# Kernel optimization log

Hardware: AMD Instinct MI355X
Metric: run time of the kernel (lower is better)

Reference implementation:

```python
import jax, jax.numpy as jnp
import numpy as np

N_HEADS = 64 * 4 // 32  # 8 heads, head_dim 32
LN_EPS = 1e-5


def conv3d(x, w, b):
    # x: [B,C,D,H,W], w: [O,I,3,3,3], padding=1 == SAME for k=3
    y = jax.lax.conv_general_dilated(
        x, w, window_strides=(1, 1, 1), padding='SAME',
        dimension_numbers=('NCDHW', 'OIDHW', 'NCDHW'))
    return y + b[None, :, None, None, None]


def layer_norm(x, g, b):
    m = jnp.mean(x, axis=-1, keepdims=True)
    v = jnp.var(x, axis=-1, keepdims=True)  # biased var, as torch LayerNorm
    return (x - m) * jax.lax.rsqrt(v + LN_EPS) * g + b


def linear(x, w, b):
    # torch Linear layout: w [out, in]
    return jnp.einsum('bsi,oi->bso', x, w) + b


def setup_inputs() -> dict:
    key = jax.random.key(0)
    ks = jax.random.split(key, 16)
    C_in, d = 64, 256
    x = jax.random.normal(ks[0], (1, C_in, 16, 16, 16), dtype=jnp.float32)
    s = 0.02
    params = {
        'conv1_w': jax.random.normal(ks[1], (d, C_in, 3, 3, 3), jnp.float32) * s,
        'conv1_b': jnp.zeros((d,), jnp.float32),
        'ln_g': jnp.ones((d,), jnp.float32),
        'ln_b': jnp.zeros((d,), jnp.float32),
        'q_w': jax.random.normal(ks[2], (d, d), jnp.float32) * s,
        'q_b': jnp.zeros((d,), jnp.float32),
        'k_w': jax.random.normal(ks[3], (d, d), jnp.float32) * s,
        'k_b': jnp.zeros((d,), jnp.float32),
        'v_w': jax.random.normal(ks[4], (d, d), jnp.float32) * s,
        'v_b': jnp.zeros((d,), jnp.float32),
        'ffn_w': jax.random.normal(ks[5], (d, d), jnp.float32) * s,
        'ffn_b': jnp.zeros((d,), jnp.float32),
        'conv2_w': jax.random.normal(ks[6], (C_in, d, 3, 3, 3), jnp.float32) * s,
        'conv2_b': jnp.zeros((C_in,), jnp.float32),
    }
    return {'x': x, **params}


def reference(x, conv1_w, conv1_b, ln_g, ln_b, q_w, q_b, k_w, k_b, v_w, v_b,
              ffn_w, ffn_b, conv2_w, conv2_b):
    B, _, D, H, W = x.shape
    S = D * H * W
    # PositionalEmbedding: conv3d then flatten; the learned pos-emb is a
    # freshly-initialized zeros Parameter in the original => no-op add.
    h0 = conv3d(x, conv1_w, conv1_b)              # [B, d, D, H, W]
    d_model = h0.shape[1]
    h0 = h0.reshape(B, d_model, S).transpose(0, 2, 1)  # [B, S, d]

    hn = layer_norm(h0, ln_g, ln_b)
    hd = d_model // N_HEADS

    def split_heads(t):
        return t.reshape(B, S, N_HEADS, hd).transpose(0, 2, 1, 3)  # [B, nH, S, hd]

    q = split_heads(linear(hn, q_w, q_b))
    k = split_heads(linear(hn, k_w, k_b))
    v = split_heads(linear(hn, v_w, v_b))

    scores = jnp.einsum('bhqd,bhkd->bhqk', q, k) / jnp.sqrt(
        jnp.asarray(hd, q.dtype))
    # NOTE: original uses nn.Softmax(dim=2) -> normalize over QUERY axis
    attn = jax.nn.softmax(scores, axis=2)
    out = jnp.einsum('bhqk,bhkd->bhqd', attn, v)  # [B, nH, S, hd]
    out = out.transpose(0, 2, 1, 3).reshape(B, S, d_model)

    xt = out + hn                                  # residual onto NORMED input
    h2 = layer_norm(xt, ln_g, ln_b)                # same LN weights reused
    h3 = jax.nn.relu(linear(h2, ffn_w, ffn_b)) + xt

    h3 = h3.transpose(0, 2, 1).reshape(B, d_model, D, H, W)
    return conv3d(h3, conv2_w, conv2_b)
```

## Files before the change

### kernel.cpp

```cpp
#include <hip/hip_runtime.h>
#include <math.h>

#define S 4096
#define DM 256

using short8 = __attribute__((ext_vector_type(8))) short;
using short4v = __attribute__((ext_vector_type(4))) short;
using f32x4 = __attribute__((ext_vector_type(4))) float;
using f32x16 = __attribute__((ext_vector_type(16))) float;

static constexpr float QK_SCALE_LOG2E = 0.17677669529663687f * 1.4426950408889634f;

__device__ __forceinline__ short f2bf(float f) {
  union { float f; unsigned u; } v;
  v.f = f;
  unsigned r = (v.u + 0x7FFFu + ((v.u >> 16) & 1u)) >> 16;
  return (short)r;
}

__device__ __forceinline__ float bf2f(short s) {
  union { unsigned u; float f; } v;
  v.u = ((unsigned)(unsigned short)s) << 16;
  return v.f;
}

__device__ __forceinline__ unsigned cvt_pk_bf16(float lo, float hi) {
  unsigned r;
  asm("v_cvt_pk_bf16_f32 %0, %1, %2" : "=v"(r) : "v"(lo), "v"(hi));
  return r;
}

__device__ __forceinline__ float fexp2(float x) {
  float r;
  asm("v_exp_f32 %0, %1" : "=v"(r) : "v"(x));
  return r;
}

__device__ __forceinline__ int pad_idx(int s) {
  int d = s >> 8, h = (s >> 4) & 15, w = s & 15;
  return ((d + 1) * 18 + (h + 1)) * 18 + (w + 1);
}

__global__ __launch_bounds__(256) void k_prep(const float* __restrict__ x,
                                              const float* __restrict__ c1w,
                                              const float* __restrict__ c2w,
                                              const float* __restrict__ qw,
                                              const float* __restrict__ kw,
                                              const float* __restrict__ vw,
                                              const float* __restrict__ fw,
                                              short* __restrict__ xpad,
                                              short* __restrict__ w1t,
                                              short* __restrict__ w2t,
                                              short* __restrict__ wqkvf,
                                              short* __restrict__ hpad) {
  int bid = blockIdx.x, tid = threadIdx.x;
  if (bid < 1458) {
    int idx = bid * 256 + tid;
    int row = idx >> 6, c = idx & 63;
    int pd = row / 324, rem = row - pd * 324;
    int ph = rem / 18, pw = rem - ph * 18;
    short v = 0;
    if ((unsigned)(pd - 1) < 16u && (unsigned)(ph - 1) < 16u && (unsigned)(pw - 1) < 16u) {
      int s = (pd - 1) * 256 + (ph - 1) * 16 + (pw - 1);
      v = f2bf(x[c * 4096 + s]);
    }
    xpad[idx] = v;
  } else if (bid < 3186) {
    int idx = (bid - 1458) * 256 + tid;
    int o = idx / 1728, r = idx - o * 1728;
    int off = r >> 6, ic = r & 63;
    w1t[idx] = f2bf(c1w[(o * 64 + ic) * 27 + off]);
  } else if (bid < 4914) {
    int idx = (bid - 3186) * 256 + tid;
    int o = idx / 6912, r = idx - o * 6912;
    int off = r >> 8, ic = r & 255;
    w2t[idx] = f2bf(c2w[(o * 256 + ic) * 27 + off]);
  } else if (bid < 5938) {
    int idx = (bid - 4914) * 256 + tid;
    int which = idx >> 16, r = idx & 65535;
    const float* src = (which == 0) ? qw : (which == 1) ? kw : (which == 2) ? vw : fw;
    wqkvf[idx] = f2bf(src[r]);
  } else {
    int i = (bid - 5938) * 2048 + tid * 8;
    short8 z = {0, 0, 0, 0, 0, 0, 0, 0};
    *(short8*)(hpad + i) = z;
  }
}

__global__ __launch_bounds__(256) void k_conv1m(const short* __restrict__ xpad,
                                                const short* __restrict__ wt,
                                                const float* __restrict__ bias,
                                                float* __restrict__ h0) {
  int bid = blockIdx.x;
  int mt2 = bid >> 1, ch = bid & 1;
  int tid = threadIdx.x, w = tid >> 6, lane = tid & 63, g = lane >> 4, c = lane & 15;
  int d = mt2 >> 3, h = (mt2 & 7) * 2;
  int nb = ch * 128 + w * 32;
  f32x4 accA0 = {}, accA1 = {}, accB0 = {}, accB1 = {};
  for (int off = 0; off < 27; ++off) {
    int kd = off / 9, r = off - kd * 9, kh = r / 3, kw = r - kh * 3;
    int rowb = ((d + kd) * 18 + h + kh) * 18 + kw + c;
#pragma unroll
    for (int kc = 0; kc < 2; ++kc) {
      short8 afA = *(const short8*)(xpad + rowb * 64 + kc * 32 + 8 * g);
      short8 afB = *(const short8*)(xpad + (rowb + 18) * 64 + kc * 32 + 8 * g);
      int kidx = off * 64 + kc * 32 + 8 * g;
      short8 b0 = *(const short8*)(wt + (nb + c) * 1728 + kidx);
      short8 b1 = *(const short8*)(wt + (nb + 16 + c) * 1728 + kidx);
      accA0 = __builtin_amdgcn_mfma_f32_16x16x32_bf16(afA, b0, accA0, 0, 0, 0);
      accA1 = __builtin_amdgcn_mfma_f32_16x16x32_bf16(afA, b1, accA1, 0, 0, 0);
      accB0 = __builtin_amdgcn_mfma_f32_16x16x32_bf16(afB, b0, accB0, 0, 0, 0);
      accB1 = __builtin_amdgcn_mfma_f32_16x16x32_bf16(afB, b1, accB1, 0, 0, 0);
    }
  }
  int o0 = nb + c, o1 = nb + 16 + c;
  float bv0 = bias[o0], bv1 = bias[o1];
  int sA = mt2 * 32 + 4 * g;
#pragma unroll
  for (int i = 0; i < 4; ++i) {
    h0[(sA + i) * 256 + o0] = accA0[i] + bv0;
    h0[(sA + i) * 256 + o1] = accA1[i] + bv1;
    h0[(sA + 16 + i) * 256 + o0] = accB0[i] + bv0;
    h0[(sA + 16 + i) * 256 + o1] = accB1[i] + bv1;
  }
}

__global__ __launch_bounds__(256) void k_layernorm(const float* __restrict__ in,
                                                   const float* __restrict__ g,
                                                   const float* __restrict__ b,
                                                   float* __restrict__ outf,
                                                   short* __restrict__ outb) {
  int s = blockIdx.x, tid = threadIdx.x;
  float xv = in[s * 256 + tid];
  float s1 = xv, s2 = xv * xv;
#pragma unroll
  for (int off = 32; off > 0; off >>= 1) {
    s1 += __shfl_down(s1, off);
    s2 += __shfl_down(s2, off);
  }
  __shared__ float w1[4], w2[4], mb[2];
  int wid = tid >> 6;
  if ((tid & 63) == 0) { w1[wid] = s1; w2[wid] = s2; }
  __syncthreads();
  if (tid == 0) {
    float t1 = w1[0] + w1[1] + w1[2] + w1[3];
    float t2 = w2[0] + w2[1] + w2[2] + w2[3];
    float m = t1 * (1.f / 256.f);
    float var = t2 * (1.f / 256.f) - m * m;
    mb[0] = m;
    mb[1] = rsqrtf(var + 1e-5f);
  }
  __syncthreads();
  float y = (xv - mb[0]) * mb[1] * g[tid] + b[tid];
  outf[s * 256 + tid] = y;
  outb[s * 256 + tid] = f2bf(y);
}

__global__ __launch_bounds__(256) void k_gemm_qkv(const short* __restrict__ ab,
                                                  const short* __restrict__ wqb,
                                                  const short* __restrict__ wkb,
                                                  const short* __restrict__ wvb,
                                                  const float* __restrict__ qbi,
                                                  const float* __restrict__ kbi,
                                                  const float* __restrict__ vbi,
                                                  short* __restrict__ qb,
                                                  short* __restrict__ kb,
                                                  short* __restrict__ vt) {
  int y = blockIdx.y;
  const short* wb = (y == 0) ? wqb : ((y == 1) ? wkb : wvb);
  int tid = threadIdx.x, w = tid >> 6, lane = tid & 63, g = lane >> 4, c = lane & 15;
  int m0 = blockIdx.x * 16;
  int nb = w * 64;
  f32x4 acc[4];
#pragma unroll
  for (int n = 0; n < 4; ++n) acc[n] = {0.f, 0.f, 0.f, 0.f};
#pragma unroll 2
  for (int k0 = 0; k0 < 256; k0 += 32) {
    short8 af = *(const short8*)(ab + (m0 + c) * 256 + k0 + 8 * g);
#pragma unroll
    for (int n = 0; n < 4; ++n) {
      short8 bf = *(const short8*)(wb + (nb + 16 * n + c) * 256 + k0 + 8 * g);
      acc[n] = __builtin_amdgcn_mfma_f32_16x16x32_bf16(af, bf, acc[n], 0, 0, 0);
    }
  }
  if (y < 2) {
    const float* bi = (y == 0) ? qbi : kbi;
    float sc = (y == 0) ? QK_SCALE_LOG2E : 1.f;
    short* ob = (y == 0) ? qb : kb;
#pragma unroll
    for (int n = 0; n < 4; ++n) {
      int o = nb + 16 * n + c;
      float bv = bi[o];
      int hh = o >> 5, dj = o & 31;
#pragma unroll
      for (int i = 0; i < 4; ++i) {
        int s = m0 + 4 * g + i;
        ob[((size_t)hh * S + s) * 32 + dj] = f2bf((acc[n][i] + bv) * sc);
      }
    }
  } else {
#pragma unroll
    for (int n = 0; n < 4; ++n) {
      int o = nb + 16 * n + c;
      float bv = vbi[o];
      short4v st;
#pragma unroll
      for (int i = 0; i < 4; ++i) st[i] = f2bf(acc[n][i] + bv);
      *(short4v*)(vt + (size_t)o * S + m0 + 4 * g) = st;
    }
  }
}

__global__ __launch_bounds__(256) void k_attn1(const short* __restrict__ qb,
                                               const short* __restrict__ kb,
                                               float* __restrict__ lpart) {
  int bid = blockIdx.x;
  int h = bid & 7;
  int rest = bid >> 3;
  int kt = rest >> 3, qs = rest & 7;
  int tid = threadIdx.x;
  int w = tid >> 6, lane = tid & 63;
  int lo = lane & 31, hi = lane >> 5;
  int k0 = kt * 128 + w * 32;
  const size_t hb = (size_t)h * S;
  const short* krow = kb + (hb + k0 + lo) * 32;
  short8 ak0 = *(const short8*)(krow + 8 * hi);
  short8 ak1 = *(const short8*)(krow + 16 + 8 * hi);
  f32x16 ls = {};
  const f32x16 z16 = {};
  int qend = qs * 512 + 512;
  for (int q0 = qs * 512; q0 < qend; q0 += 32) {
    short8 bq0 = *(const short8*)(qb + (hb + q0 + lo) * 32 + 8 * hi);
    short8 bq1 = *(const short8*)(qb + (hb + q0 + lo) * 32 + 16 + 8 * hi);
    __builtin_amdgcn_s_setprio(1);
    f32x16 p = __builtin_amdgcn_mfma_f32_32x32x16_bf16(ak0, bq0, z16, 0, 0, 0);
    p = __builtin_amdgcn_mfma_f32_32x32x16_bf16(ak1, bq1, p, 0, 0, 0);
    __builtin_amdgcn_s_setprio(0);
#pragma unroll
    for (int r = 0; r < 16; ++r) ls[r] += fexp2(p[r]);
  }
#pragma unroll
  for (int r = 0; r < 16; ++r) {
    float v = ls[r];
    v += __shfl_xor(v, 1);
    v += __shfl_xor(v, 2);
    v += __shfl_xor(v, 4);
    v += __shfl_xor(v, 8);
    v += __shfl_xor(v, 16);
    ls[r] = v;
  }
  if (lo == 0) {
#pragma unroll
    for (int r = 0; r < 16; ++r)
      lpart[qs * 32768 + h * 4096 + k0 + (r & 3) + 8 * (r >> 2) + 4 * hi] = ls[r];
  }
}

__global__ __launch_bounds__(256) void k_scalevt(short* __restrict__ vt,
                                                 const float* __restrict__ lpart) {
  int idx = blockIdx.x * 256 + threadIdx.x;
  int row = idx >> 9;
  int col0 = (idx & 511) << 3;
  int h = row >> 5;
  const float* lp = lpart + h * 4096 + col0;
  float4 s0 = {0.f, 0.f, 0.f, 0.f}, s1 = {0.f, 0.f, 0.f, 0.f};
#pragma unroll
  for (int j = 0; j < 8; ++j) {
    float4 a = *(const float4*)(lp + j * 32768);
    float4 b = *(const float4*)(lp + j * 32768 + 4);
    s0.x += a.x; s0.y += a.y; s0.z += a.z; s0.w += a.w;
    s1.x += b.x; s1.y += b.y; s1.z += b.z; s1.w += b.w;
  }
  float4 l0, l1;
  l0.x = 1.f / s0.x; l0.y = 1.f / s0.y; l0.z = 1.f / s0.z; l0.w = 1.f / s0.w;
  l1.x = 1.f / s1.x; l1.y = 1.f / s1.y; l1.z = 1.f / s1.z; l1.w = 1.f / s1.w;
  short8 v = *(short8*)(vt + (size_t)row * S + col0);
  union { unsigned u[4]; short8 s8; } r;
  r.u[0] = cvt_pk_bf16(bf2f(v[0]) * l0.x, bf2f(v[1]) * l0.y);
  r.u[1] = cvt_pk_bf16(bf2f(v[2]) * l0.z, bf2f(v[3]) * l0.w);
  r.u[2] = cvt_pk_bf16(bf2f(v[4]) * l1.x, bf2f(v[5]) * l1.y);
  r.u[3] = cvt_pk_bf16(bf2f(v[6]) * l1.z, bf2f(v[7]) * l1.w);
  *(short8*)(vt + (size_t)row * S + col0) = r.s8;
}

__global__ __launch_bounds__(256, 4) void k_attn2(const short* __restrict__ qb,
                                                  const short* __restrict__ kb,
                                                  const short* __restrict__ vt,
                                                  short* __restrict__ parts) {
  int bid = blockIdx.x;
  int h = bid & 7;
  int rest = bid >> 3;
  int qt = rest >> 3, ks = rest & 7;
  int tid = threadIdx.x;
  int w = tid >> 6, lane = tid & 63;
  int lo = lane & 31, hi = lane >> 5;
  int sl = lo ^ ((((lo >> 2) ^ (lo >> 3)) & 1) * 12);
  int q0a = qt * 256 + w * 64;
  int q0b = q0a + 32;
  const size_t hb = (size_t)h * S;
  short8 bqa0 = *(const short8*)(qb + (hb + q0a + lo) * 32 + 8 * hi);
  short8 bqa1 = *(const short8*)(qb + (hb + q0a + lo) * 32 + 16 + 8 * hi);
  short8 bqb0 = *(const short8*)(qb + (hb + q0b + lo) * 32 + 8 * hi);
  short8 bqb1 = *(const short8*)(qb + (hb + q0b + lo) * 32 + 16 + 8 * hi);
  f32x16 accA = {}, accB = {};
  const short* krow = kb + (hb + sl) * 32;
  const short* vrow = vt + ((size_t)(h * 32) + lo) * S;
  const f32x16 z16 = {};
  int k0 = ks * 512;
  short8 ak0 = *(const short8*)(krow + (size_t)k0 * 32 + 8 * hi);
  short8 ak1 = *(const short8*)(krow + (size_t)k0 * 32 + 16 + 8 * hi);
#pragma unroll 1
  for (int it = 0; it < 16; ++it) {
    int kn = k0 + 32;
    short8 nak0 = *(const short8*)(krow + (size_t)kn * 32 + 8 * hi);
    short8 nak1 = *(const short8*)(krow + (size_t)kn * 32 + 16 + 8 * hi);
    short8 bv0 = *(const short8*)(vrow + k0 + 8 * hi);
    short8 bv1 = *(const short8*)(vrow + k0 + 16 + 8 * hi);
    __builtin_amdgcn_s_setprio(1);
    f32x16 pA = __builtin_amdgcn_mfma_f32_32x32x16_bf16(ak0, bqa0, z16, 0, 0, 0);
    f32x16 pB = __builtin_amdgcn_mfma_f32_32x32x16_bf16(ak0, bqb0, z16, 0, 0, 0);
    pA = __builtin_amdgcn_mfma_f32_32x32x16_bf16(ak1, bqa1, pA, 0, 0, 0);
    pB = __builtin_amdgcn_mfma_f32_32x32x16_bf16(ak1, bqb1, pB, 0, 0, 0);
    __builtin_amdgcn_s_setprio(0);
    union { unsigned u[4]; short8 s8; } fA0, fA1, fB0, fB1;
#pragma unroll
    for (int m = 0; m < 4; ++m)
      fA0.u[m] = cvt_pk_bf16(fexp2(pA[2 * m]), fexp2(pA[2 * m + 1]));
#pragma unroll
    for (int m = 0; m < 4; ++m)
      fA1.u[m] = cvt_pk_bf16(fexp2(pA[8 + 2 * m]), fexp2(pA[9 + 2 * m]));
#pragma unroll
    for (int m = 0; m < 4; ++m)
      fB0.u[m] = cvt_pk_bf16(fexp2(pB[2 * m]), fexp2(pB[2 * m + 1]));
#pragma unroll
    for (int m = 0; m < 4; ++m)
      fB1.u[m] = cvt_pk_bf16(fexp2(pB[8 + 2 * m]), fexp2(pB[9 + 2 * m]));
    __builtin_amdgcn_s_setprio(1);
    accA = __builtin_amdgcn_mfma_f32_32x32x16_bf16(fA0.s8, bv0, accA, 0, 0, 0);
    accB = __builtin_amdgcn_mfma_f32_32x32x16_bf16(fB0.s8, bv0, accB, 0, 0, 0);
    accA = __builtin_amdgcn_mfma_f32_32x32x16_bf16(fA1.s8, bv1, accA, 0, 0, 0);
    accB = __builtin_amdgcn_mfma_f32_32x32x16_bf16(fB1.s8, bv1, accB, 0, 0, 0);
    __builtin_amdgcn_s_setprio(0);
    ak0 = nak0;
    ak1 = nak1;
    k0 = kn;
  }
  short* part = parts + (size_t)ks * (S * DM);
  int col = h * 32 + lo;
#pragma unroll
  for (int r = 0; r < 16; ++r) {
    int qrel = (r & 3) + 8 * (r >> 2) + 4 * hi;
    part[(q0a + qrel) * 256 + col] = f2bf(accA[r]);
    part[(q0b + qrel) * 256 + col] = f2bf(accB[r]);
  }
}

__global__ __launch_bounds__(256) void k_combine_ln(const short* __restrict__ parts,
                                                    const float* __restrict__ hn,
                                                    const float* __restrict__ g,
                                                    const float* __restrict__ b,
                                                    float* __restrict__ xt,
                                                    short* __restrict__ h2b) {
  int s = blockIdx.x, tid = threadIdx.x;
  int i = s * 256 + tid;
  const int SD4 = S * DM;
  float xv = hn[i];
#pragma unroll
  for (int j = 0; j < 8; ++j) xv += bf2f(parts[i + j * SD4]);
  xt[i] = xv;
  float s1 = xv, s2 = xv * xv;
#pragma unroll
  for (int off = 32; off > 0; off >>= 1) {
    s1 += __shfl_down(s1, off);
    s2 += __shfl_down(s2, off);
  }
  __shared__ float w1[4], w2[4], mb[2];
  int wid = tid >> 6;
  if ((tid & 63) == 0) { w1[wid] = s1; w2[wid] = s2; }
  __syncthreads();
  if (tid == 0) {
    float t1 = w1[0] + w1[1] + w1[2] + w1[3];
    float t2 = w2[0] + w2[1] + w2[2] + w2[3];
    float m = t1 * (1.f / 256.f);
    float var = t2 * (1.f / 256.f) - m * m;
    mb[0] = m;
    mb[1] = rsqrtf(var + 1e-5f);
  }
  __syncthreads();
  h2b[i] = f2bf((xv - mb[0]) * mb[1] * g[tid] + b[tid]);
}

__global__ __launch_bounds__(256) void k_gemm_ffn(const short* __restrict__ ab,
                                                  const short* __restrict__ wb,
                                                  const float* __restrict__ bi,
                                                  const float* __restrict__ xt,
                                                  short* __restrict__ hpad) {
  int tid = threadIdx.x, w = tid >> 6, lane = tid & 63, g = lane >> 4, c = lane & 15;
  int m0 = blockIdx.x * 16;
  int nb = w * 64;
  f32x4 acc[4];
#pragma unroll
  for (int n = 0; n < 4; ++n) acc[n] = {0.f, 0.f, 0.f, 0.f};
#pragma unroll 2
  for (int k0 = 0; k0 < 256; k0 += 32) {
    short8 af = *(const short8*)(ab + (m0 + c) * 256 + k0 + 8 * g);
#pragma unroll
    for (int n = 0; n < 4; ++n) {
      short8 bf = *(const short8*)(wb + (nb + 16 * n + c) * 256 + k0 + 8 * g);
      acc[n] = __builtin_amdgcn_mfma_f32_16x16x32_bf16(af, bf, acc[n], 0, 0, 0);
    }
  }
  int pr[4];
#pragma unroll
  for (int i = 0; i < 4; ++i) pr[i] = pad_idx(m0 + 4 * g + i) * 256;
#pragma unroll
  for (int n = 0; n < 4; ++n) {
    int o = nb + 16 * n + c;
    float bv = bi[o];
#pragma unroll
    for (int i = 0; i < 4; ++i) {
      int s = m0 + 4 * g + i;
      float v = acc[n][i] + bv;
      v = v > 0.f ? v : 0.f;
      hpad[pr[i] + o] = f2bf(v + xt[s * 256 + o]);
    }
  }
}

__global__ __launch_bounds__(256) void k_conv2m(const short* __restrict__ hpad,
                                                const short* __restrict__ wt,
                                                float* __restrict__ pbase) {
  __shared__ float red[3][32][65];
  int bid = blockIdx.x;
  int mt2 = bid >> 2, kh = bid & 3;
  int tid = threadIdx.x, w = tid >> 6, lane = tid & 63, g = lane >> 4, c = lane & 15;
  int d = mt2 >> 3, h = (mt2 & 7) * 2;
  f32x4 accA[4], accB[4];
#pragma unroll
  for (int n = 0; n < 4; ++n) { accA[n] = {0.f, 0.f, 0.f, 0.f}; accB[n] = {0.f, 0.f, 0.f, 0.f}; }
  int off0 = kh * 7;
  int offn = (kh == 3) ? 6 : 7;
  for (int off = off0 + w; off < off0 + offn; off += 4) {
    int kd = off / 9, rr = off - kd * 9, kkh = rr / 3, kw = rr - kkh * 3;
    int rowb = ((d + kd) * 18 + h + kkh) * 18 + kw + c;
    const short* arowA = hpad + rowb * 256;
    const short* arowB = hpad + (rowb + 18) * 256;
    const short* wrow = wt + off * 256;
#pragma unroll 2
    for (int kc = 0; kc < 8; ++kc) {
      short8 afA = *(const short8*)(arowA + kc * 32 + 8 * g);
      short8 afB = *(const short8*)(arowB + kc * 32 + 8 * g);
#pragma unroll
      for (int n = 0; n < 4; ++n) {
        short8 bf = *(const short8*)(wrow + (16 * n + c) * 6912 + kc * 32 + 8 * g);
        accA[n] = __builtin_amdgcn_mfma_f32_16x16x32_bf16(afA, bf, accA[n], 0, 0, 0);
        accB[n] = __builtin_amdgcn_mfma_f32_16x16x32_bf16(afB, bf, accB[n], 0, 0, 0);
      }
    }
  }
  if (w > 0) {
#pragma unroll
    for (int n = 0; n < 4; ++n)
#pragma unroll
      for (int i = 0; i < 4; ++i) {
        red[w - 1][n * 4 + i][lane] = accA[n][i];
        red[w - 1][16 + n * 4 + i][lane] = accB[n][i];
      }
  }
  __syncthreads();
  if (w == 0) {
    float* pbuf = pbase + (size_t)kh * (S * DM / 4);
#pragma unroll
    for (int n = 0; n < 4; ++n) {
      int o = 16 * n + c;
      float4 stA, stB;
#pragma unroll
      for (int i = 0; i < 4; ++i) {
        float a = accA[n][i] + red[0][n * 4 + i][lane] + red[1][n * 4 + i][lane] + red[2][n * 4 + i][lane];
        float bb = accB[n][i] + red[0][16 + n * 4 + i][lane] + red[1][16 + n * 4 + i][lane] + red[2][16 + n * 4 + i][lane];
        ((float*)&stA)[i] = a;
        ((float*)&stB)[i] = bb;
      }
      *(float4*)(pbuf + o * 4096 + mt2 * 32 + 4 * g) = stA;
      *(float4*)(pbuf + o * 4096 + mt2 * 32 + 16 + 4 * g) = stB;
    }
  }
}

__global__ __launch_bounds__(256) void k_conv2fin(const float* __restrict__ pbase,
                                                  const float* __restrict__ bias,
                                                  float* __restrict__ out) {
  int idx4 = (blockIdx.x * 256 + threadIdx.x) * 4;
  int o = idx4 >> 12;
  const int PS = S * DM / 4;
  float4 a = *(const float4*)(pbase + idx4);
  float4 b = *(const float4*)(pbase + PS + idx4);
  float4 c = *(const float4*)(pbase + 2 * PS + idx4);
  float4 d = *(const float4*)(pbase + 3 * PS + idx4);
  float bv = bias[o];
  float4 r;
  r.x = a.x + b.x + c.x + d.x + bv;
  r.y = a.y + b.y + c.y + d.y + bv;
  r.z = a.z + b.z + c.z + d.z + bv;
  r.w = a.w + b.w + c.w + d.w + bv;
  *(float4*)(out + idx4) = r;
}

extern "C" void kernel_launch(void* const* d_in, const int* in_sizes, int n_in,
                              void* d_out, int out_size, void* d_ws, size_t ws_size,
                              hipStream_t stream) {
  const float* x   = (const float*)d_in[0];
  const float* c1w = (const float*)d_in[1];
  const float* c1b = (const float*)d_in[2];
  const float* lng = (const float*)d_in[3];
  const float* lnb = (const float*)d_in[4];
  const float* qw  = (const float*)d_in[5];
  const float* qbi = (const float*)d_in[6];
  const float* kw  = (const float*)d_in[7];
  const float* kbi = (const float*)d_in[8];
  const float* vw  = (const float*)d_in[9];
  const float* vbi = (const float*)d_in[10];
  const float* fw  = (const float*)d_in[11];
  const float* fbi = (const float*)d_in[12];
  const float* c2w = (const float*)d_in[13];
  const float* c2b = (const float*)d_in[14];
  float* out = (float*)d_out;
  float* ws = (float*)d_ws;

  const size_t SD = (size_t)S * DM;
  float* hn     = ws;
  float* xt     = hn + SD;
  short* partsb = (short*)(xt + SD);
  float* h0     = (float*)partsb;
  float* c2p    = (float*)partsb;
  float* lpart  = (float*)(partsb + 8 * SD);
  float* linv   = lpart + 262144;
  short* hnb    = (short*)(linv + 32768);
  short* h2b    = hnb + SD;
  short* qb     = h2b + SD;
  short* kb     = qb + SD;
  short* vt     = kb + SD;
  short* xpad   = vt + SD;
  short* hpad   = xpad + 373248;
  short* w1t    = hpad + 1492992;
  short* w2t    = w1t + 442368;
  short* wqb    = w2t + 442368;
  short* wkb    = wqb + 65536;
  short* wvb    = wkb + 65536;
  short* wfb    = wvb + 65536;

  k_prep<<<6667, 256, 0, stream>>>(x, c1w, c2w, qw, kw, vw, fw,
                                   xpad, w1t, w2t, wqb, hpad);

  k_conv1m<<<256, 256, 0, stream>>>(xpad, w1t, c1b, h0);
  k_layernorm<<<4096, 256, 0, stream>>>(h0, lng, lnb, hn, hnb);

  k_gemm_qkv<<<dim3(256, 3), 256, 0, stream>>>(hnb, wqb, wkb, wvb, qbi, kbi, vbi,
                                               qb, kb, vt);

  k_attn1<<<2048, 256, 0, stream>>>(qb, kb, lpart);
  k_scalevt<<<1024, 256, 0, stream>>>(vt, lpart);
  k_attn2<<<1024, 256, 0, stream>>>(qb, kb, vt, partsb);
  k_combine_ln<<<4096, 256, 0, stream>>>(partsb, hn, lng, lnb, xt, h2b);

  k_gemm_ffn<<<256, 256, 0, stream>>>(h2b, wfb, fbi, xt, hpad);
  k_conv2m<<<512, 256, 0, stream>>>(hpad, w2t, c2p);
  k_conv2fin<<<256, 256, 0, stream>>>(c2p, c2b, out);
}
```

Before: 151.0 us.

## Fuse conv1 with LayerNorm and transpose conv weights through LDS

Conv1 is retiled so each block computes all 256 output channels for 16 spatial rows. This lets the LayerNorm mean and variance be reduced in-block and applied before writing hn/hnb, which removes the separate LayerNorm kernel and the fp32 h0 round trip. Weight prep now uses one block per output channel that reads the source contiguously and transposes through shared memory, cutting the prep grid size. The cost is less reuse of each A fragment per block (16 rows instead of 32) and fewer blocks in conv1, since one block now covers 16 rows by 256 channels.

Result: slower. 154.2 us (+2.1%).

```diff
diff --git a/kernel.cpp b/kernel.cpp
--- a/kernel.cpp
+++ b/kernel.cpp
@@ -53,6 +53,7 @@
                                               short* __restrict__ w2t,
                                               short* __restrict__ wqkvf,
                                               short* __restrict__ hpad) {
+  __shared__ short tlds[6912];
   int bid = blockIdx.x, tid = threadIdx.x;
   if (bid < 1458) {
     int idx = bid * 256 + tid;
@@ -65,95 +66,114 @@
       v = f2bf(x[c * 4096 + s]);
     }
     xpad[idx] = v;
-  } else if (bid < 3186) {
-    int idx = (bid - 1458) * 256 + tid;
-    int o = idx / 1728, r = idx - o * 1728;
-    int off = r >> 6, ic = r & 63;
-    w1t[idx] = f2bf(c1w[(o * 64 + ic) * 27 + off]);
-  } else if (bid < 4914) {
-    int idx = (bid - 3186) * 256 + tid;
-    int o = idx / 6912, r = idx - o * 6912;
-    int off = r >> 8, ic = r & 255;
-    w2t[idx] = f2bf(c2w[(o * 256 + ic) * 27 + off]);
-  } else if (bid < 5938) {
-    int idx = (bid - 4914) * 256 + tid;
+  } else if (bid < 1714) {
+    int o = bid - 1458;
+    const float* src = c1w + o * 1728;
+    for (int t = tid; t < 1728; t += 256) {
+      int ic = t / 27, off = t - ic * 27;
+      tlds[off * 64 + ic] = f2bf(src[t]);
+    }
+    __syncthreads();
+    for (int u = tid; u < 1728; u += 256) w1t[o * 1728 + u] = tlds[u];
+  } else if (bid < 1778) {
+    int o = bid - 1714;
+    const float* src = c2w + o * 6912;
+    for (int t = tid; t < 6912; t += 256) {
+      int ic = t / 27, off = t - ic * 27;
+      tlds[off * 256 + ic] = f2bf(src[t]);
+    }
+    __syncthreads();
+    for (int u = tid; u < 6912; u += 256) w2t[o * 6912 + u] = tlds[u];
+  } else if (bid < 2802) {
+    int idx = (bid - 1778) * 256 + tid;
     int which = idx >> 16, r = idx & 65535;
     const float* src = (which == 0) ? qw : (which == 1) ? kw : (which == 2) ? vw : fw;
     wqkvf[idx] = f2bf(src[r]);
   } else {
-    int i = (bid - 5938) * 2048 + tid * 8;
+    int i = (bid - 2802) * 2048 + tid * 8;
     short8 z = {0, 0, 0, 0, 0, 0, 0, 0};
     *(short8*)(hpad + i) = z;
   }
 }
 
-__global__ __launch_bounds__(256) void k_conv1m(const short* __restrict__ xpad,
-                                                const short* __restrict__ wt,
-                                                const float* __restrict__ bias,
-                                                float* __restrict__ h0) {
-  int bid = blockIdx.x;
-  int mt2 = bid >> 1, ch = bid & 1;
+__global__ __launch_bounds__(256) void k_conv1ln(const short* __restrict__ xpad,
+                                                 const short* __restrict__ wt,
+                                                 const float* __restrict__ bias,
+                                                 const float* __restrict__ lng,
+                                                 const float* __restrict__ lnb,
+                                                 float* __restrict__ hn,
+                                                 short* __restrict__ hnb) {
+  __shared__ float red1[4][16], red2[4][16];
+  __shared__ float mstd[16][2];
+  int mt = blockIdx.x;
   int tid = threadIdx.x, w = tid >> 6, lane = tid & 63, g = lane >> 4, c = lane & 15;
-  int d = mt2 >> 3, h = (mt2 & 7) * 2;
-  int nb = ch * 128 + w * 32;
-  f32x4 accA0 = {}, accA1 = {}, accB0 = {}, accB1 = {};
+  int d = mt >> 4, h = mt & 15;
+  int nb = w * 64;
+  f32x4 acc[4];
+#pragma unroll
+  for (int n = 0; n < 4; ++n) acc[n] = {0.f, 0.f, 0.f, 0.f};
   for (int off = 0; off < 27; ++off) {
     int kd = off / 9, r = off - kd * 9, kh = r / 3, kw = r - kh * 3;
     int rowb = ((d + kd) * 18 + h + kh) * 18 + kw + c;
 #pragma unroll
     for (int kc = 0; kc < 2; ++kc) {
-      short8 afA = *(const short8*)(xpad + rowb * 64 + kc * 32 + 8 * g);
-      short8 afB = *(const short8*)(xpad + (rowb + 18) * 64 + kc * 32 + 8 * g);
+      short8 af = *(const short8*)(xpad + rowb * 64 + kc * 32 + 8 * g);
       int kidx = off * 64 + kc * 32 + 8 * g;
-      short8 b0 = *(const short8*)(wt + (nb + c) * 1728 + kidx);
-      short8 b1 = *(const short8*)(wt + (nb + 16 + c) * 1728 + kidx);
-      accA0 = __builtin_amdgcn_mfma_f32_16x16x32_bf16(afA, b0, accA0, 0, 0, 0);
-      accA1 = __builtin_amdgcn_mfma_f32_16x16x32_bf16(afA, b1, accA1, 0, 0, 0);
-      accB0 = __builtin_amdgcn_mfma_f32_16x16x32_bf16(afB, b0, accB0, 0, 0, 0);
-      accB1 = __builtin_amdgcn_mfma_f32_16x16x32_bf16(afB, b1, accB1, 0, 0, 0);
-    }
-  }
-  int o0 = nb + c, o1 = nb + 16 + c;
-  float bv0 = bias[o0], bv1 = bias[o1];
-  int sA = mt2 * 32 + 4 * g;
+#pragma unroll
+      for (int n = 0; n < 4; ++n) {
+        short8 bf = *(const short8*)(wt + (nb + 16 * n + c) * 1728 + kidx);
+        acc[n] = __builtin_amdgcn_mfma_f32_16x16x32_bf16(af, bf, acc[n], 0, 0, 0);
+      }
+    }
+  }
+  float s1[4] = {0.f, 0.f, 0.f, 0.f}, s2[4] = {0.f, 0.f, 0.f, 0.f};
+#pragma unroll
+  for (int n = 0; n < 4; ++n) {
+    float bv = bias[nb + 16 * n + c];
+#pragma unroll
+    for (int i = 0; i < 4; ++i) {
+      acc[n][i] += bv;
+      s1[i] += acc[n][i];
+      s2[i] += acc[n][i] * acc[n][i];
+    }
+  }
 #pragma unroll
   for (int i = 0; i < 4; ++i) {
-    h0[(sA + i) * 256 + o0] = accA0[i] + bv0;
-    h0[(sA + i) * 256 + o1] = accA1[i] + bv1;
-    h0[(sA + 16 + i) * 256 + o0] = accB0[i] + bv0;
-    h0[(sA + 16 + i) * 256 + o1] = accB1[i] + bv1;
-  }
-}
-
-__global__ __launch_bounds__(256) void k_layernorm(const float* __restrict__ in,
-                                                   const float* __restrict__ g,
-                                                   const float* __restrict__ b,
-                                                   float* __restrict__ outf,
-                                                   short* __restrict__ outb) {
-  int s = blockIdx.x, tid = threadIdx.x;
-  float xv = in[s * 256 + tid];
-  float s1 = xv, s2 = xv * xv;
-#pragma unroll
-  for (int off = 32; off > 0; off >>= 1) {
-    s1 += __shfl_down(s1, off);
-    s2 += __shfl_down(s2, off);
-  }
-  __shared__ float w1[4], w2[4], mb[2];
-  int wid = tid >> 6;
-  if ((tid & 63) == 0) { w1[wid] = s1; w2[wid] = s2; }
+    s1[i] += __shfl_xor(s1[i], 1); s2[i] += __shfl_xor(s2[i], 1);
+    s1[i] += __shfl_xor(s1[i], 2); s2[i] += __shfl_xor(s2[i], 2);
+    s1[i] += __shfl_xor(s1[i], 4); s2[i] += __shfl_xor(s2[i], 4);
+    s1[i] += __shfl_xor(s1[i], 8); s2[i] += __shfl_xor(s2[i], 8);
+  }
+  if (c == 0) {
+#pragma unroll
+    for (int i = 0; i < 4; ++i) {
+      red1[w][4 * g + i] = s1[i];
+      red2[w][4 * g + i] = s2[i];
+    }
+  }
   __syncthreads();
-  if (tid == 0) {
-    float t1 = w1[0] + w1[1] + w1[2] + w1[3];
-    float t2 = w2[0] + w2[1] + w2[2] + w2[3];
+  if (tid < 16) {
+    float t1 = red1[0][tid] + red1[1][tid] + red1[2][tid] + red1[3][tid];
+    float t2 = red2[0][tid] + red2[1][tid] + red2[2][tid] + red2[3][tid];
     float m = t1 * (1.f / 256.f);
     float var = t2 * (1.f / 256.f) - m * m;
-    mb[0] = m;
-    mb[1] = rsqrtf(var + 1e-5f);
+    mstd[tid][0] = m;
+    mstd[tid][1] = rsqrtf(var + 1e-5f);
   }
   __syncthreads();
-  float y = (xv - mb[0]) * mb[1] * g[tid] + b[tid];
-  outf[s * 256 + tid] = y;
-  outb[s * 256 + tid] = f2bf(y);
+  int s0 = mt * 16;
+#pragma unroll
+  for (int n = 0; n < 4; ++n) {
+    int o = nb + 16 * n + c;
+    float gg = lng[o], bb = lnb[o];
+#pragma unroll
+    for (int i = 0; i < 4; ++i) {
+      int row = 4 * g + i;
+      float y = (acc[n][i] - mstd[row][0]) * mstd[row][1] * gg + bb;
+      hn[(s0 + row) * 256 + o] = y;
+      hnb[(s0 + row) * 256 + o] = f2bf(y);
+    }
+  }
 }
 
 __global__ __launch_bounds__(256) void k_gemm_qkv(const short* __restrict__ ab,
@@ -531,7 +551,6 @@
   float* hn     = ws;
   float* xt     = hn + SD;
   short* partsb = (short*)(xt + SD);
-  float* h0     = (float*)partsb;
   float* c2p    = (float*)partsb;
   float* lpart  = (float*)(partsb + 8 * SD);
   float* linv   = lpart + 262144;
@@ -549,11 +568,10 @@
   short* wvb    = wkb + 65536;
   short* wfb    = wvb + 65536;
 
-  k_prep<<<6667, 256, 0, stream>>>(x, c1w, c2w, qw, kw, vw, fw,
+  k_prep<<<3531, 256, 0, stream>>>(x, c1w, c2w, qw, kw, vw, fw,
                                    xpad, w1t, w2t, wqb, hpad);
 
-  k_conv1m<<<256, 256, 0, stream>>>(xpad, w1t, c1b, h0);
-  k_layernorm<<<4096, 256, 0, stream>>>(h0, lng, lnb, hn, hnb);
+  k_conv1ln<<<256, 256, 0, stream>>>(xpad, w1t, c1b, lng, lnb, hn, hnb);
 
   k_gemm_qkv<<<dim3(256, 3), 256, 0, stream>>>(hnb, wqb, wkb, wvb, qbi, kbi, vbi,
                                                qb, kb, vt);
```

## Fuse layernorms into QKV and FFN GEMMs and transpose conv weights via LDS

Applied to the files above, without the earlier changes.

Drops the standalone layernorm and combine-layernorm kernels. The QKV GEMM now computes LN1 from h0 into swizzled LDS before its MFMA loop. A new FFN kernel recomputes LN1, adds the 8 attention partials, applies LN2 and keeps xt in LDS for the residual. Conv weight reordering in the prep kernel now goes through an LDS transpose with one block per output channel, which cuts the prep grid size. This removes two launches and the fp32/bf16 round-trips of hn, xt, hnb and h2b, at the cost of recomputing LN1 three times per row across QKV blocks and once more in the FFN kernel.

Result: faster. 143.2 us (-5.2%).

```diff
diff --git a/kernel.cpp b/kernel.cpp
--- a/kernel.cpp
+++ b/kernel.cpp
@@ -53,6 +53,7 @@
                                               short* __restrict__ w2t,
                                               short* __restrict__ wqkvf,
                                               short* __restrict__ hpad) {
+  __shared__ short tlds[7128];
   int bid = blockIdx.x, tid = threadIdx.x;
   if (bid < 1458) {
     int idx = bid * 256 + tid;
@@ -65,23 +66,37 @@
       v = f2bf(x[c * 4096 + s]);
     }
     xpad[idx] = v;
-  } else if (bid < 3186) {
-    int idx = (bid - 1458) * 256 + tid;
-    int o = idx / 1728, r = idx - o * 1728;
-    int off = r >> 6, ic = r & 63;
-    w1t[idx] = f2bf(c1w[(o * 64 + ic) * 27 + off]);
-  } else if (bid < 4914) {
-    int idx = (bid - 3186) * 256 + tid;
-    int o = idx / 6912, r = idx - o * 6912;
-    int off = r >> 8, ic = r & 255;
-    w2t[idx] = f2bf(c2w[(o * 256 + ic) * 27 + off]);
-  } else if (bid < 5938) {
-    int idx = (bid - 4914) * 256 + tid;
+  } else if (bid < 1714) {
+    int o = bid - 1458;
+    const float* src = c1w + o * 1728;
+    for (int t = tid; t < 1728; t += 256) {
+      int ic = t / 27, off = t - ic * 27;
+      tlds[off * 72 + ic] = f2bf(src[t]);
+    }
+    __syncthreads();
+    for (int u = tid; u < 1728; u += 256) {
+      int off = u >> 6, ic = u & 63;
+      w1t[o * 1728 + u] = tlds[off * 72 + ic];
+    }
+  } else if (bid < 1778) {
+    int o = bid - 1714;
+    const float* src = c2w + o * 6912;
+    for (int t = tid; t < 6912; t += 256) {
+      int ic = t / 27, off = t - ic * 27;
+      tlds[off * 264 + ic] = f2bf(src[t]);
+    }
+    __syncthreads();
+    for (int u = tid; u < 6912; u += 256) {
+      int off = u >> 8, ic = u & 255;
+      w2t[o * 6912 + u] = tlds[off * 264 + ic];
+    }
+  } else if (bid < 2802) {
+    int idx = (bid - 1778) * 256 + tid;
     int which = idx >> 16, r = idx & 65535;
     const float* src = (which == 0) ? qw : (which == 1) ? kw : (which == 2) ? vw : fw;
     wqkvf[idx] = f2bf(src[r]);
   } else {
-    int i = (bid - 5938) * 2048 + tid * 8;
+    int i = (bid - 2802) * 2048 + tid * 8;
     short8 z = {0, 0, 0, 0, 0, 0, 0, 0};
     *(short8*)(hpad + i) = z;
   }
@@ -125,38 +140,9 @@
   }
 }
 
-__global__ __launch_bounds__(256) void k_layernorm(const float* __restrict__ in,
-                                                   const float* __restrict__ g,
-                                                   const float* __restrict__ b,
-                                                   float* __restrict__ outf,
-                                                   short* __restrict__ outb) {
-  int s = blockIdx.x, tid = threadIdx.x;
-  float xv = in[s * 256 + tid];
-  float s1 = xv, s2 = xv * xv;
-#pragma unroll
-  for (int off = 32; off > 0; off >>= 1) {
-    s1 += __shfl_down(s1, off);
-    s2 += __shfl_down(s2, off);
-  }
-  __shared__ float w1[4], w2[4], mb[2];
-  int wid = tid >> 6;
-  if ((tid & 63) == 0) { w1[wid] = s1; w2[wid] = s2; }
-  __syncthreads();
-  if (tid == 0) {
-    float t1 = w1[0] + w1[1] + w1[2] + w1[3];
-    float t2 = w2[0] + w2[1] + w2[2] + w2[3];
-    float m = t1 * (1.f / 256.f);
-    float var = t2 * (1.f / 256.f) - m * m;
-    mb[0] = m;
-    mb[1] = rsqrtf(var + 1e-5f);
-  }
-  __syncthreads();
-  float y = (xv - mb[0]) * mb[1] * g[tid] + b[tid];
-  outf[s * 256 + tid] = y;
-  outb[s * 256 + tid] = f2bf(y);
-}
-
-__global__ __launch_bounds__(256) void k_gemm_qkv(const short* __restrict__ ab,
+__global__ __launch_bounds__(256) void k_gemm_qkv(const float* __restrict__ h0,
+                                                  const float* __restrict__ lng,
+                                                  const float* __restrict__ lnb,
                                                   const short* __restrict__ wqb,
                                                   const short* __restrict__ wkb,
                                                   const short* __restrict__ wvb,
@@ -166,17 +152,62 @@
                                                   short* __restrict__ qb,
                                                   short* __restrict__ kb,
                                                   short* __restrict__ vt) {
+  __shared__ short h2l[4096];
+  int m0 = blockIdx.x * 16;
+  int tid = threadIdx.x;
+  {
+    int r = tid >> 4, cg = tid & 15;
+    int row = m0 + r;
+    float u[16];
+    const float* hp = h0 + row * 256 + cg * 16;
+#pragma unroll
+    for (int i = 0; i < 16; i += 4) {
+      float4 a = *(const float4*)(hp + i);
+      u[i] = a.x; u[i + 1] = a.y; u[i + 2] = a.z; u[i + 3] = a.w;
+    }
+    float s1 = 0.f, s2 = 0.f;
+#pragma unroll
+    for (int i = 0; i < 16; ++i) { s1 += u[i]; s2 += u[i] * u[i]; }
+    s1 += __shfl_xor(s1, 1); s2 += __shfl_xor(s2, 1);
+    s1 += __shfl_xor(s1, 2); s2 += __shfl_xor(s2, 2);
+    s1 += __shfl_xor(s1, 4); s2 += __shfl_xor(s2, 4);
+    s1 += __shfl_xor(s1, 8); s2 += __shfl_xor(s2, 8);
+    float m = s1 * (1.f / 256.f);
+    float rstd = rsqrtf(s2 * (1.f / 256.f) - m * m + 1e-5f);
+    float gv[16], bv[16];
+#pragma unroll
+    for (int i = 0; i < 16; i += 4) {
+      float4 a = *(const float4*)(lng + cg * 16 + i);
+      float4 b = *(const float4*)(lnb + cg * 16 + i);
+      gv[i] = a.x; gv[i + 1] = a.y; gv[i + 2] = a.z; gv[i + 3] = a.w;
+      bv[i] = b.x; bv[i + 1] = b.y; bv[i + 2] = b.z; bv[i + 3] = b.w;
+    }
+    union { unsigned uu[4]; short8 s8; } o0, o1;
+#pragma unroll
+    for (int i = 0; i < 8; i += 2) {
+      float y0 = (u[i] - m) * rstd * gv[i] + bv[i];
+      float y1 = (u[i + 1] - m) * rstd * gv[i + 1] + bv[i + 1];
+      o0.uu[i >> 1] = cvt_pk_bf16(y0, y1);
+      float y8 = (u[8 + i] - m) * rstd * gv[8 + i] + bv[8 + i];
+      float y9 = (u[9 + i] - m) * rstd * gv[9 + i] + bv[9 + i];
+      o1.uu[i >> 1] = cvt_pk_bf16(y8, y9);
+    }
+    char* base = (char*)h2l;
+    *(short8*)(base + ((r * 512 + cg * 32) ^ ((r & 7) << 4))) = o0.s8;
+    *(short8*)(base + ((r * 512 + cg * 32 + 16) ^ ((r & 7) << 4))) = o1.s8;
+  }
+  __syncthreads();
   int y = blockIdx.y;
   const short* wb = (y == 0) ? wqb : ((y == 1) ? wkb : wvb);
-  int tid = threadIdx.x, w = tid >> 6, lane = tid & 63, g = lane >> 4, c = lane & 15;
-  int m0 = blockIdx.x * 16;
+  int w = tid >> 6, lane = tid & 63, g = lane >> 4, c = lane & 15;
   int nb = w * 64;
   f32x4 acc[4];
 #pragma unroll
   for (int n = 0; n < 4; ++n) acc[n] = {0.f, 0.f, 0.f, 0.f};
+  const char* abase = (const char*)h2l;
 #pragma unroll 2
   for (int k0 = 0; k0 < 256; k0 += 32) {
-    short8 af = *(const short8*)(ab + (m0 + c) * 256 + k0 + 8 * g);
+    short8 af = *(const short8*)(abase + ((c * 512 + (k0 + 8 * g) * 2) ^ ((c & 7) << 4)));
 #pragma unroll
     for (int n = 0; n < 4; ++n) {
       short8 bf = *(const short8*)(wb + (nb + 16 * n + c) * 256 + k0 + 8 * g);
@@ -190,22 +221,22 @@
 #pragma unroll
     for (int n = 0; n < 4; ++n) {
       int o = nb + 16 * n + c;
-      float bv = bi[o];
+      float bvv = bi[o];
       int hh = o >> 5, dj = o & 31;
 #pragma unroll
       for (int i = 0; i < 4; ++i) {
         int s = m0 + 4 * g + i;
-        ob[((size_t)hh * S + s) * 32 + dj] = f2bf((acc[n][i] + bv) * sc);
+        ob[((size_t)hh * S + s) * 32 + dj] = f2bf((acc[n][i] + bvv) * sc);
       }
     }
   } else {
 #pragma unroll
     for (int n = 0; n < 4; ++n) {
       int o = nb + 16 * n + c;
-      float bv = vbi[o];
+      float bvv = vbi[o];
       short4v st;
 #pragma unroll
-      for (int i = 0; i < 4; ++i) st[i] = f2bf(acc[n][i] + bv);
+      for (int i = 0; i < 4; ++i) st[i] = f2bf(acc[n][i] + bvv);
       *(short4v*)(vt + (size_t)o * S + m0 + 4 * g) = st;
     }
   }
@@ -355,55 +386,95 @@
   }
 }
 
-__global__ __launch_bounds__(256) void k_combine_ln(const short* __restrict__ parts,
-                                                    const float* __restrict__ hn,
-                                                    const float* __restrict__ g,
-                                                    const float* __restrict__ b,
-                                                    float* __restrict__ xt,
-                                                    short* __restrict__ h2b) {
-  int s = blockIdx.x, tid = threadIdx.x;
-  int i = s * 256 + tid;
-  const int SD4 = S * DM;
-  float xv = hn[i];
-#pragma unroll
-  for (int j = 0; j < 8; ++j) xv += bf2f(parts[i + j * SD4]);
-  xt[i] = xv;
-  float s1 = xv, s2 = xv * xv;
-#pragma unroll
-  for (int off = 32; off > 0; off >>= 1) {
-    s1 += __shfl_down(s1, off);
-    s2 += __shfl_down(s2, off);
-  }
-  __shared__ float w1[4], w2[4], mb[2];
-  int wid = tid >> 6;
-  if ((tid & 63) == 0) { w1[wid] = s1; w2[wid] = s2; }
+__global__ __launch_bounds__(256) void k_ffn_fused(const float* __restrict__ h0,
+                                                   const short* __restrict__ parts,
+                                                   const float* __restrict__ lng,
+                                                   const float* __restrict__ lnb,
+                                                   const short* __restrict__ wb,
+                                                   const float* __restrict__ bi,
+                                                   short* __restrict__ hpad) {
+  __shared__ short h2l[4096];
+  __shared__ float xtl[16][256];
+  int m0 = blockIdx.x * 16;
+  int tid = threadIdx.x;
+  {
+    int r = tid >> 4, cg = tid & 15;
+    int row = m0 + r;
+    float u[16];
+    const float* hp = h0 + row * 256 + cg * 16;
+#pragma unroll
+    for (int i = 0; i < 16; i += 4) {
+      float4 a = *(const float4*)(hp + i);
+      u[i] = a.x; u[i + 1] = a.y; u[i + 2] = a.z; u[i + 3] = a.w;
+    }
+    float s1 = 0.f, s2 = 0.f;
+#pragma unroll
+    for (int i = 0; i < 16; ++i) { s1 += u[i]; s2 += u[i] * u[i]; }
+    s1 += __shfl_xor(s1, 1); s2 += __shfl_xor(s2, 1);
+    s1 += __shfl_xor(s1, 2); s2 += __shfl_xor(s2, 2);
+    s1 += __shfl_xor(s1, 4); s2 += __shfl_xor(s2, 4);
+    s1 += __shfl_xor(s1, 8); s2 += __shfl_xor(s2, 8);
+    float m1 = s1 * (1.f / 256.f);
+    float rstd1 = rsqrtf(s2 * (1.f / 256.f) - m1 * m1 + 1e-5f);
+    float gv[16], bvv[16];
+#pragma unroll
+    for (int i = 0; i < 16; i += 4) {
+      float4 a = *(const float4*)(lng + cg * 16 + i);
+      float4 b = *(const float4*)(lnb + cg * 16 + i);
+      gv[i] = a.x; gv[i + 1] = a.y; gv[i + 2] = a.z; gv[i + 3] = a.w;
+      bvv[i] = b.x; bvv[i + 1] = b.y; bvv[i + 2] = b.z; bvv[i + 3] = b.w;
+    }
+    float xv[16];
+#pragma unroll
+    for (int i = 0; i < 16; ++i) xv[i] = (u[i] - m1) * rstd1 * gv[i] + bvv[i];
+    const int SD4 = S * DM;
+#pragma unroll
+    for (int j = 0; j < 8; ++j) {
+      const short* pp = parts + j * SD4 + row * 256 + cg * 16;
+      short8 p0 = *(const short8*)(pp);
+      short8 p1 = *(const short8*)(pp + 8);
+#pragma unroll
+      for (int i = 0; i < 8; ++i) { xv[i] += bf2f(p0[i]); xv[8 + i] += bf2f(p1[i]); }
+    }
+    s1 = 0.f; s2 = 0.f;
+#pragma unroll
+    for (int i = 0; i < 16; ++i) { s1 += xv[i]; s2 += xv[i] * xv[i]; }
+    s1 += __shfl_xor(s1, 1); s2 += __shfl_xor(s2, 1);
+    s1 += __shfl_xor(s1, 2); s2 += __shfl_xor(s2, 2);
+    s1 += __shfl_xor(s1, 4); s2 += __shfl_xor(s2, 4);
+    s1 += __shfl_xor(s1, 8); s2 += __shfl_xor(s2, 8);
+    float m2 = s1 * (1.f / 256.f);
+    float rstd2 = rsqrtf(s2 * (1.f / 256.f) - m2 * m2 + 1e-5f);
+#pragma unroll
+    for (int i = 0; i < 16; i += 4) {
+      float4 a;
+      a.x = xv[i]; a.y = xv[i + 1]; a.z = xv[i + 2]; a.w = xv[i + 3];
+      *(float4*)(&xtl[r][cg * 16 + i]) = a;
+    }
+    union { unsigned uu[4]; short8 s8; } o0, o1;
+#pragma unroll
+    for (int i = 0; i < 8; i += 2) {
+      float y0 = (xv[i] - m2) * rstd2 * gv[i] + bvv[i];
+      float y1 = (xv[i + 1] - m2) * rstd2 * gv[i + 1] + bvv[i + 1];
+      o0.uu[i >> 1] = cvt_pk_bf16(y0, y1);
+      float y8 = (xv[8 + i] - m2) * rstd2 * gv[8 + i] + bvv[8 + i];
+      float y9 = (xv[9 + i] - m2) * rstd2 * gv[9 + i] + bvv[9 + i];
+      o1.uu[i >> 1] = cvt_pk_bf16(y8, y9);
+    }
+    char* base = (char*)h2l;
+    *(short8*)(base + ((r * 512 + cg * 32) ^ ((r & 7) << 4))) = o0.s8;
+    *(short8*)(base + ((r * 512 + cg * 32 + 16) ^ ((r & 7) << 4))) = o1.s8;
+  }
   __syncthreads();
-  if (tid == 0) {
-    float t1 = w1[0] + w1[1] + w1[2] + w1[3];
-    float t2 = w2[0] + w2[1] + w2[2] + w2[3];
-    float m = t1 * (1.f / 256.f);
-    float var = t2 * (1.f / 256.f) - m * m;
-    mb[0] = m;
-    mb[1] = rsqrtf(var + 1e-5f);
-  }
-  __syncthreads();
-  h2b[i] = f2bf((xv - mb[0]) * mb[1] * g[tid] + b[tid]);
-}
-
-__global__ __launch_bounds__(256) void k_gemm_ffn(const short* __restrict__ ab,
-                                                  const short* __restrict__ wb,
-                                                  const float* __restrict__ bi,
-                                                  const float* __restrict__ xt,
-                                                  short* __restrict__ hpad) {
-  int tid = threadIdx.x, w = tid >> 6, lane = tid & 63, g = lane >> 4, c = lane & 15;
-  int m0 = blockIdx.x * 16;
+  int w = tid >> 6, lane = tid & 63, g = lane >> 4, c = lane & 15;
   int nb = w * 64;
   f32x4 acc[4];
 #pragma unroll
   for (int n = 0; n < 4; ++n) acc[n] = {0.f, 0.f, 0.f, 0.f};
+  const char* abase = (const char*)h2l;
 #pragma unroll 2
   for (int k0 = 0; k0 < 256; k0 += 32) {
-    short8 af = *(const short8*)(ab + (m0 + c) * 256 + k0 + 8 * g);
+    short8 af = *(const short8*)(abase + ((c * 512 + (k0 + 8 * g) * 2) ^ ((c & 7) << 4)));
 #pragma unroll
     for (int n = 0; n < 4; ++n) {
       short8 bf = *(const short8*)(wb + (nb + 16 * n + c) * 256 + k0 + 8 * g);
@@ -416,13 +487,12 @@
 #pragma unroll
   for (int n = 0; n < 4; ++n) {
     int o = nb + 16 * n + c;
-    float bv = bi[o];
+    float bvv = bi[o];
 #pragma unroll
     for (int i = 0; i < 4; ++i) {
-      int s = m0 + 4 * g + i;
-      float v = acc[n][i] + bv;
+      float v = acc[n][i] + bvv;
       v = v > 0.f ? v : 0.f;
-      hpad[pr[i] + o] = f2bf(v + xt[s * 256 + o]);
+      hpad[pr[i] + o] = f2bf(v + xtl[4 * g + i][o]);
     }
   }
 }
@@ -528,16 +598,11 @@
   float* ws = (float*)d_ws;
 
   const size_t SD = (size_t)S * DM;
-  float* hn     = ws;
-  float* xt     = hn + SD;
-  short* partsb = (short*)(xt + SD);
-  float* h0     = (float*)partsb;
+  float* h0     = ws;
+  short* partsb = (short*)(h0 + SD);
   float* c2p    = (float*)partsb;
   float* lpart  = (float*)(partsb + 8 * SD);
-  float* linv   = lpart + 262144;
-  short* hnb    = (short*)(linv + 32768);
-  short* h2b    = hnb + SD;
-  short* qb     = h2b + SD;
+  short* qb     = (short*)(lpart + 262144);
   short* kb     = qb + SD;
   short* vt     = kb + SD;
   short* xpad   = vt + SD;
@@ -549,21 +614,20 @@
   short* wvb    = wkb + 65536;
   short* wfb    = wvb + 65536;
 
-  k_prep<<<6667, 256, 0, stream>>>(x, c1w, c2w, qw, kw, vw, fw,
+  k_prep<<<3531, 256, 0, stream>>>(x, c1w, c2w, qw, kw, vw, fw,
                                    xpad, w1t, w2t, wqb, hpad);
 
   k_conv1m<<<256, 256, 0, stream>>>(xpad, w1t, c1b, h0);
-  k_layernorm<<<4096, 256, 0, stream>>>(h0, lng, lnb, hn, hnb);
-
-  k_gemm_qkv<<<dim3(256, 3), 256, 0, stream>>>(hnb, wqb, wkb, wvb, qbi, kbi, vbi,
-                                               qb, kb, vt);
+
+  k_gemm_qkv<<<dim3(256, 3), 256, 0, stream>>>(h0, lng, lnb, wqb, wkb, wvb,
+                                               qbi, kbi, vbi, qb, kb, vt);
 
   k_attn1<<<2048, 256, 0, stream>>>(qb, kb, lpart);
   k_scalevt<<<1024, 256, 0, stream>>>(vt, lpart);
   k_attn2<<<1024, 256, 0, stream>>>(qb, kb, vt, partsb);
-  k_combine_ln<<<4096, 256, 0, stream>>>(partsb, hn, lng, lnb, xt, h2b);
-
-  k_gemm_ffn<<<256, 256, 0, stream>>>(h2b, wfb, fbi, xt, hpad);
+
+  k_ffn_fused<<<256, 256, 0, stream>>>(h0, partsb, lng, lnb, wfb, fbi, hpad);
+
   k_conv2m<<<512, 256, 0, stream>>>(hpad, w2t, c2p);
   k_conv2fin<<<256, 256, 0, stream>>>(c2p, c2b, out);
 }
```
